# Kernel optimization log

Measured on AMD Instinct MI355X. Metric: run time of the kernel, lower is better.

The kernel has to match this reference:

```python
import jax, jax.numpy as jnp
import numpy as np

IN_F, OUT_F = 64, 32
N = IN_F * OUT_F + OUT_F  # 2080 sampled parameters (weights + bias)
B, S = 8, 2048
SCALE_INIT = 1.0 * float(np.sqrt(2.0 / (IN_F + OUT_F)))


def setup_inputs() -> dict:
    key = jax.random.key(0)
    k_x, k_eps, k_loc, k_cov = jax.random.split(key, 4)
    x = jax.random.normal(k_x, (B, S, IN_F), dtype=jnp.float32)
    eps = jax.random.normal(k_eps, (B, S, N), dtype=jnp.float32)
    loc = 0.01 * jax.random.normal(k_loc, (N,), dtype=jnp.float32)
    logvar = jnp.full((N,), float(np.log(SCALE_INIT)), dtype=jnp.float32)
    n_off = N * (N - 1) // 2
    cov_flat = 0.001 * jax.random.normal(k_cov, (n_off,), dtype=jnp.float32)
    return {"x": x, "eps": eps, "loc": loc, "logvar": logvar, "cov_flat": cov_flat}


def reference(x, eps, loc, logvar, cov_flat):
    n = loc.shape[0]
    in_f = x.shape[-1]
    out_f = n // (in_f + 1)  # n = out*(in+1)
    # flat_to_triangular (strictly lower) + make_cholesky, vectorized scatter
    rows, cols = np.tril_indices(n, -1)
    A = jnp.zeros((n, n), dtype=x.dtype).at[rows, cols].set(cov_flat)
    L = A + jnp.diag(jnp.exp(logvar * 0.5))  # off-diag from cov, diag = std
    # MultivariateNormal rsample: loc + L @ eps (per batch sample)
    W = loc + jnp.einsum('bsn,mn->bsm', eps, L)  # [B,S,N]
    b = W[..., :out_f]
    Wm = W[..., out_f:].reshape(*W.shape[:-1], in_f, out_f)  # [B,S,in,out]
    y = jnp.einsum('bsh,bshk->bsk', x, Wm) + b
    return y
```

## Files before the change

kernel.cpp:

```cpp
#include <hip/hip_runtime.h>
#include <hip/hip_bf16.h>

#define IN_F  64
#define OUT_F 32
#define NV    2080
#define NPAD  2176
#define MM    16384
#define KK    2080
#define NBN   17
#define BM    256

typedef __attribute__((ext_vector_type(4))) float f32x4;
typedef __bf16 bf16x8 __attribute__((ext_vector_type(8)));

using gas_ptr = const __attribute__((address_space(1))) void*;
using lds_ptr = __attribute__((address_space(3))) void*;

__global__ __launch_bounds__(256) void build_L_k(const float* __restrict__ cov,
                                                 const float* __restrict__ logvar,
                                                 __hip_bfloat16* __restrict__ LB) {
    const int idx = blockIdx.x * 256 + threadIdx.x;
    const int m = idx / KK;
    const int k = idx - m * KK;
    float v = 0.0f;
    if (m < NV) {
        if (k < m)       v = cov[(size_t)(m * (m - 1) / 2) + k];
        else if (k == m) v = expf(0.5f * logvar[m]);
    }
    LB[idx] = __float2bfloat16(v);
}

__global__ __launch_bounds__(256, 2) void gemm_v3_k(const float* __restrict__ A,
                                                    const __hip_bfloat16* __restrict__ BT,
                                                    const float* __restrict__ loc,
                                                    const float* __restrict__ x,
                                                    float* __restrict__ Ypart) {
    __shared__ __align__(16) __hip_bfloat16 As[2][BM * 32];
    __shared__ __align__(16) __hip_bfloat16 Bs[3][128 * 32];
    __shared__ float xs[BM][4];

    const int tid  = threadIdx.x;
    const int bm   = blockIdx.x;
    const int bn   = (NBN - 1) - blockIdx.y;
    const int wave = tid >> 6;
    const int lane = tid & 63;
    const int quad = lane >> 4;
    const int r16  = lane & 15;
    const int kblocks = min(KK / 32, 4 * bn + 4);

    {
        const int row = bm * BM + tid;
#pragma unroll
        for (int c = 0; c < 4; c++) {
            const int h = 4 * bn - 1 + c;
            float w = 0.0f;
            if (bn == 0 && c == 0)       w = 1.0f;
            else if (h >= 0 && h < IN_F) w = x[(size_t)row * IN_F + h];
            xs[tid][c] = w;
        }
    }

    const float*          __restrict__ Ag = A  + (size_t)bm * BM * KK;
    const __hip_bfloat16* __restrict__ Bg = BT + (size_t)bn * 128 * KK;

    size_t agofs[4]; int aldso[4];
#pragma unroll
    for (int u = 0; u < 4; u++) {
        const int c = tid + 256 * u;
        const int r = c >> 2, p = (c & 3) ^ ((r >> 1) & 3);
        agofs[u] = (size_t)r * KK + (size_t)(p * 8);
        aldso[u] = c * 8;
    }
    size_t bgofs[2]; int bldso[2];
#pragma unroll
    for (int u = 0; u < 2; u++) {
        const int c = tid + 256 * u;
        const int r = c >> 2, p = (c & 3) ^ ((r >> 1) & 3);
        bgofs[u] = (size_t)r * KK + (size_t)(p * 8);
        bldso[u] = c * 8;
    }

    int aofs[4], bofs[8];
#pragma unroll
    for (int i = 0; i < 4; i++) {
        const int arow = 64 * wave + 16 * i + r16;
        aofs[i] = arow * 32 + (quad ^ ((arow >> 1) & 3)) * 8;
    }
#pragma unroll
    for (int j = 0; j < 8; j++) {
        const int brow = 16 * j + r16;
        bofs[j] = brow * 32 + (quad ^ ((brow >> 1) & 3)) * 8;
    }

    f32x4 acc[4][8];
#pragma unroll
    for (int i = 0; i < 4; i++)
#pragma unroll
        for (int j = 0; j < 8; j++) acc[i][j] = f32x4{0.f, 0.f, 0.f, 0.f};

    f32x4 ra[8];

    auto loadA = [&](int t) __attribute__((always_inline)) {
        const size_t k0 = (size_t)t * 32;
#pragma unroll
        for (int u = 0; u < 4; u++) {
            ra[2 * u]     = *(const f32x4*)(Ag + k0 + agofs[u]);
            ra[2 * u + 1] = *(const f32x4*)(Ag + k0 + agofs[u] + 4);
        }
    };
    auto writeA = [&](int buf) __attribute__((always_inline)) {
#pragma unroll
        for (int u = 0; u < 4; u++) {
            bf16x8 w;
#pragma unroll
            for (int q = 0; q < 4; q++) {
                w[q]     = (__bf16)ra[2 * u][q];
                w[4 + q] = (__bf16)ra[2 * u + 1][q];
            }
            *(bf16x8*)(&As[buf][0] + aldso[u]) = w;
        }
    };
    auto stageB = [&](int t, int buf) __attribute__((always_inline)) {
        const size_t k0 = (size_t)t * 32;
#pragma unroll
        for (int u = 0; u < 2; u++)
            __builtin_amdgcn_global_load_lds((gas_ptr)(Bg + k0 + bgofs[u]),
                                             (lds_ptr)(&Bs[buf][0] + bldso[u]), 16, 0, 0);
    };

    loadA(0);
    __builtin_amdgcn_sched_barrier(0);
    stageB(0, 0);
    stageB(1, 1);
    __builtin_amdgcn_sched_barrier(0);
    writeA(0);
    loadA(1);
    __builtin_amdgcn_sched_barrier(0);
    asm volatile("s_waitcnt vmcnt(10)" ::: "memory");
    asm volatile("s_waitcnt lgkmcnt(0)" ::: "memory");
    __builtin_amdgcn_s_barrier();
    __builtin_amdgcn_sched_barrier(0);

    auto iter = [&](int t, int jlo) __attribute__((always_inline)) {
        const bool pfA = (t + 1 < kblocks);
        const bool pfB = (t + 2 < kblocks);
        if (pfB) stageB(t + 2, (t + 2) % 3);
        const __hip_bfloat16* as = &As[t & 1][0];
        const __hip_bfloat16* bs = &Bs[t % 3][0];
        bf16x8 af[4];
#pragma unroll
        for (int i = 0; i < 4; i++) af[i] = *(const bf16x8*)(as + aofs[i]);
        __builtin_amdgcn_s_setprio(1);
#pragma unroll
        for (int j = 0; j < 8; j++) {
            if (j >= jlo) {
                const bf16x8 bf = *(const bf16x8*)(bs + bofs[j]);
#pragma unroll
                for (int i = 0; i < 4; i++)
                    acc[i][j] = __builtin_amdgcn_mfma_f32_16x16x32_bf16(af[i], bf, acc[i][j], 0, 0, 0);
            }
        }
        __builtin_amdgcn_s_setprio(0);
        if (pfA) {
            if (pfB) { asm volatile("s_waitcnt vmcnt(2)" ::: "memory"); }
            else     { asm volatile("s_waitcnt vmcnt(0)" ::: "memory"); }
            writeA((t + 1) & 1);
            if (pfB) loadA(t + 2);
            asm volatile("s_waitcnt lgkmcnt(0)" ::: "memory");
            __builtin_amdgcn_s_barrier();
            __builtin_amdgcn_sched_barrier(0);
        }
    };

    const int t_full = min(kblocks, 4 * bn + 1);
    int t = 0;
    for (; t < t_full; ++t) iter(t, 0);
    for (; t < kblocks; ++t) iter(t, 2 * t - 8 * bn);

    float locv[8];
#pragma unroll
    for (int j = 0; j < 8; j++) {
        const int col = bn * 128 + 16 * j + r16;
        locv[j] = (col < NV) ? loc[col] : 0.0f;
    }

    float* yp = Ypart + ((size_t)bn * MM + (size_t)bm * BM) * OUT_F;
#pragma unroll
    for (int i = 0; i < 4; i++) {
#pragma unroll
        for (int r = 0; r < 4; r++) {
            const int tl = 64 * wave + 16 * i + 4 * quad + r;
            float v0 = 0.0f, v1 = 0.0f;
#pragma unroll
            for (int c = 0; c < 4; c++) {
                const float w = xs[tl][c];
                v0 += w * (acc[i][2 * c][r]     + locv[2 * c]);
                v1 += w * (acc[i][2 * c + 1][r] + locv[2 * c + 1]);
            }
            yp[(size_t)tl * OUT_F + r16]      = v0;
            yp[(size_t)tl * OUT_F + 16 + r16] = v1;
        }
    }
}

__global__ __launch_bounds__(256) void reduce_y_k(const float4* __restrict__ yp,
                                                  float4* __restrict__ y) {
    const size_t i = (size_t)blockIdx.x * 256 + threadIdx.x;
    float4 s = yp[i];
#pragma unroll
    for (int b = 1; b < NBN; b++) {
        float4 v = yp[i + (size_t)b * (MM * OUT_F / 4)];
        s.x += v.x; s.y += v.y; s.z += v.z; s.w += v.w;
    }
    y[i] = s;
}

extern "C" void kernel_launch(void* const* d_in, const int* in_sizes, int n_in,
                              void* d_out, int out_size, void* d_ws, size_t ws_size,
                              hipStream_t stream) {
    const float* x      = (const float*)d_in[0];
    const float* eps    = (const float*)d_in[1];
    const float* loc    = (const float*)d_in[2];
    const float* logvar = (const float*)d_in[3];
    const float* cov    = (const float*)d_in[4];
    float* y = (float*)d_out;

    char* ws = (char*)d_ws;
    const size_t lb_bytes = (size_t)NPAD * KK * 2;
    __hip_bfloat16* LB    = (__hip_bfloat16*)ws;
    float*          Ypart = (float*)(ws + lb_bytes);

    build_L_k<<<(NPAD * KK) / 256, 256, 0, stream>>>(cov, logvar, LB);
    gemm_v3_k<<<dim3(MM / BM, NBN), 256, 0, stream>>>(eps, LB, loc, x, Ypart);
    reduce_y_k<<<(MM * OUT_F / 4) / 256, 256, 0, stream>>>((const float4*)Ypart, (float4*)y);
}
```

Baseline: 315.6 us.

## Restructure GEMM to stream N-tiles per K-slice with fused x-weighted epilogue

After: 417.7 us. 32.3% more time.

```diff
diff --git a/kernel.cpp b/kernel.cpp
--- a/kernel.cpp
+++ b/kernel.cpp
@@ -7,7 +7,7 @@
 #define NPAD  2176
 #define MM    16384
 #define KK    2080
-#define NBN   17
+#define NTC   8
 #define BM    256
 
 typedef __attribute__((ext_vector_type(4))) float f32x4;
@@ -30,38 +30,23 @@
     LB[idx] = __float2bfloat16(v);
 }
 
-__global__ __launch_bounds__(256, 2) void gemm_v3_k(const float* __restrict__ A,
-                                                    const __hip_bfloat16* __restrict__ BT,
-                                                    const float* __restrict__ loc,
-                                                    const float* __restrict__ x,
-                                                    float* __restrict__ Ypart) {
+__global__ __launch_bounds__(256) void gemm_v4_k(const float* __restrict__ A,
+                                                 const __hip_bfloat16* __restrict__ BT,
+                                                 const float* __restrict__ loc,
+                                                 const float* __restrict__ x,
+                                                 float* __restrict__ Ypart) {
     __shared__ __align__(16) __hip_bfloat16 As[2][BM * 32];
-    __shared__ __align__(16) __hip_bfloat16 Bs[3][128 * 32];
-    __shared__ float xs[BM][4];
+    __shared__ __align__(16) __hip_bfloat16 Bs[2][128 * 32];
 
     const int tid  = threadIdx.x;
     const int bm   = blockIdx.x;
-    const int bn   = (NBN - 1) - blockIdx.y;
+    const int tc   = blockIdx.y;
     const int wave = tid >> 6;
     const int lane = tid & 63;
     const int quad = lane >> 4;
     const int r16  = lane & 15;
-    const int kblocks = min(KK / 32, 4 * bn + 4);
-
-    {
-        const int row = bm * BM + tid;
-#pragma unroll
-        for (int c = 0; c < 4; c++) {
-            const int h = 4 * bn - 1 + c;
-            float w = 0.0f;
-            if (bn == 0 && c == 0)       w = 1.0f;
-            else if (h >= 0 && h < IN_F) w = x[(size_t)row * IN_F + h];
-            xs[tid][c] = w;
-        }
-    }
-
-    const float*          __restrict__ Ag = A  + (size_t)bm * BM * KK;
-    const __hip_bfloat16* __restrict__ Bg = BT + (size_t)bn * 128 * KK;
+
+    const float* __restrict__ Ag = A + (size_t)bm * BM * KK;
 
     size_t agofs[4]; int aldso[4];
 #pragma unroll
@@ -92,11 +77,13 @@
         bofs[j] = brow * 32 + (quad ^ ((brow >> 1) & 3)) * 8;
     }
 
-    f32x4 acc[4][8];
-#pragma unroll
-    for (int i = 0; i < 4; i++)
-#pragma unroll
-        for (int j = 0; j < 8; j++) acc[i][j] = f32x4{0.f, 0.f, 0.f, 0.f};
+    int rowi[4];
+#pragma unroll
+    for (int i = 0; i < 4; i++) rowi[i] = bm * BM + 64 * wave + 16 * i + r16;
+
+    f32x4 yacc[4][2];
+#pragma unroll
+    for (int i = 0; i < 4; i++) { yacc[i][0] = f32x4{0.f,0.f,0.f,0.f}; yacc[i][1] = f32x4{0.f,0.f,0.f,0.f}; }
 
     f32x4 ra[8];
 
@@ -120,95 +107,128 @@
             *(bf16x8*)(&As[buf][0] + aldso[u]) = w;
         }
     };
-    auto stageB = [&](int t, int buf) __attribute__((always_inline)) {
-        const size_t k0 = (size_t)t * 32;
+    auto stageB = [&](int t, int bn, int buf) __attribute__((always_inline)) {
+        const __hip_bfloat16* Bg = BT + (size_t)bn * 128 * KK + (size_t)t * 32;
 #pragma unroll
         for (int u = 0; u < 2; u++)
-            __builtin_amdgcn_global_load_lds((gas_ptr)(Bg + k0 + bgofs[u]),
+            __builtin_amdgcn_global_load_lds((gas_ptr)(Bg + bgofs[u]),
                                              (lds_ptr)(&Bs[buf][0] + bldso[u]), 16, 0, 0);
     };
-
-    loadA(0);
-    __builtin_amdgcn_sched_barrier(0);
-    stageB(0, 0);
-    stageB(1, 1);
-    __builtin_amdgcn_sched_barrier(0);
+    auto loadW = [&](int bn, f32x4* w) __attribute__((always_inline)) {
+        if (bn == 0) {
+#pragma unroll
+            for (int i = 0; i < 4; i++) {
+                f32x4 v = *(const f32x4*)(x + (size_t)rowi[i] * IN_F);
+                w[i] = f32x4{1.0f, v[0], v[1], v[2]};
+            }
+        } else if (bn == 16) {
+#pragma unroll
+            for (int i = 0; i < 4; i++) {
+                float v = x[(size_t)rowi[i] * IN_F + 63];
+                w[i] = f32x4{v, 0.f, 0.f, 0.f};
+            }
+        } else {
+#pragma unroll
+            for (int i = 0; i < 4; i++)
+                w[i] = *(const f32x4*)(x + (size_t)rowi[i] * IN_F + 4 * bn - 1);
+        }
+    };
+
+    int t = tc, bn = tc >> 2;
+    loadA(t);
+    stageB(t, bn, 0);
+    f32x4 w[4];
+    loadW(bn, w);
     writeA(0);
-    loadA(1);
-    __builtin_amdgcn_sched_barrier(0);
-    asm volatile("s_waitcnt vmcnt(10)" ::: "memory");
+    asm volatile("s_waitcnt vmcnt(0)" ::: "memory");
     asm volatile("s_waitcnt lgkmcnt(0)" ::: "memory");
     __builtin_amdgcn_s_barrier();
     __builtin_amdgcn_sched_barrier(0);
 
-    auto iter = [&](int t, int jlo) __attribute__((always_inline)) {
-        const bool pfA = (t + 1 < kblocks);
-        const bool pfB = (t + 2 < kblocks);
-        if (pfB) stageB(t + 2, (t + 2) % 3);
-        const __hip_bfloat16* as = &As[t & 1][0];
-        const __hip_bfloat16* bs = &Bs[t % 3][0];
-        bf16x8 af[4];
-#pragma unroll
-        for (int i = 0; i < 4; i++) af[i] = *(const bf16x8*)(as + aofs[i]);
+    bf16x8 af[4];
+#pragma unroll
+    for (int i = 0; i < 4; i++) af[i] = *(const bf16x8*)(&As[0][0] + aofs[i]);
+    int abuf = 0, bbuf = 0;
+
+    for (;;) {
+        int t1, bn1; bool hasNext;
+        if (bn < 16) { t1 = t; bn1 = bn + 1; hasNext = true; }
+        else         { t1 = t + NTC; bn1 = t1 >> 2; hasNext = (t1 <= KK / 32 - 1); }
+        const bool stA = (bn == 16) && hasNext;
+
+        if (hasNext) stageB(t1, bn1, bbuf ^ 1);
+        f32x4 wn[4];
+        if (hasNext) loadW(bn1, wn);
+        if (stA) loadA(t1);
+
+        const bool addloc = (t == 0);
+        f32x4 lv[8];
+        if (addloc) {
+#pragma unroll
+            for (int j = 0; j < 8; j++) {
+                const int cb = 128 * bn + 16 * j + 4 * quad;
+                lv[j] = (cb < NV - 3) ? *(const f32x4*)(loc + cb) : f32x4{0.f,0.f,0.f,0.f};
+            }
+        }
+
+        const int jlo = (2 * t > 8 * bn) ? (2 * t - 8 * bn) : 0;
+        const __hip_bfloat16* bs = &Bs[bbuf][0];
         __builtin_amdgcn_s_setprio(1);
 #pragma unroll
         for (int j = 0; j < 8; j++) {
             if (j >= jlo) {
-                const bf16x8 bf = *(const bf16x8*)(bs + bofs[j]);
-#pragma unroll
-                for (int i = 0; i < 4; i++)
-                    acc[i][j] = __builtin_amdgcn_mfma_f32_16x16x32_bf16(af[i], bf, acc[i][j], 0, 0, 0);
+                const bf16x8 bfr = *(const bf16x8*)(bs + bofs[j]);
+#pragma unroll
+                for (int i = 0; i < 4; i++) {
+                    f32x4 tl = __builtin_amdgcn_mfma_f32_16x16x32_bf16(
+                                   bfr, af[i], f32x4{0.f,0.f,0.f,0.f}, 0, 0, 0);
+                    if (addloc) tl += lv[j];
+                    const float wc = w[i][j >> 1];
+                    yacc[i][j & 1] += wc * tl;
+                }
             }
         }
         __builtin_amdgcn_s_setprio(0);
-        if (pfA) {
-            if (pfB) { asm volatile("s_waitcnt vmcnt(2)" ::: "memory"); }
-            else     { asm volatile("s_waitcnt vmcnt(0)" ::: "memory"); }
-            writeA((t + 1) & 1);
-            if (pfB) loadA(t + 2);
-            asm volatile("s_waitcnt lgkmcnt(0)" ::: "memory");
-            __builtin_amdgcn_s_barrier();
-            __builtin_amdgcn_sched_barrier(0);
-        }
-    };
-
-    const int t_full = min(kblocks, 4 * bn + 1);
-    int t = 0;
-    for (; t < t_full; ++t) iter(t, 0);
-    for (; t < kblocks; ++t) iter(t, 2 * t - 8 * bn);
-
-    float locv[8];
-#pragma unroll
-    for (int j = 0; j < 8; j++) {
-        const int col = bn * 128 + 16 * j + r16;
-        locv[j] = (col < NV) ? loc[col] : 0.0f;
-    }
-
-    float* yp = Ypart + ((size_t)bn * MM + (size_t)bm * BM) * OUT_F;
+
+        if (!hasNext) break;
+
+        if (stA) {
+            asm volatile("s_waitcnt vmcnt(0)" ::: "memory");
+            writeA(abuf ^ 1);
+        } else {
+            asm volatile("s_waitcnt vmcnt(4)" ::: "memory");
+        }
+        asm volatile("s_waitcnt lgkmcnt(0)" ::: "memory");
+        __builtin_amdgcn_s_barrier();
+        __builtin_amdgcn_sched_barrier(0);
+
+        if (stA) {
+            abuf ^= 1;
+#pragma unroll
+            for (int i = 0; i < 4; i++) af[i] = *(const bf16x8*)(&As[abuf][0] + aofs[i]);
+        }
+        bbuf ^= 1;
+#pragma unroll
+        for (int i = 0; i < 4; i++) w[i] = wn[i];
+        t = t1; bn = bn1;
+    }
+
+    float* yp = Ypart + ((size_t)tc * MM + (size_t)bm * BM) * OUT_F;
 #pragma unroll
     for (int i = 0; i < 4; i++) {
-#pragma unroll
-        for (int r = 0; r < 4; r++) {
-            const int tl = 64 * wave + 16 * i + 4 * quad + r;
-            float v0 = 0.0f, v1 = 0.0f;
-#pragma unroll
-            for (int c = 0; c < 4; c++) {
-                const float w = xs[tl][c];
-                v0 += w * (acc[i][2 * c][r]     + locv[2 * c]);
-                v1 += w * (acc[i][2 * c + 1][r] + locv[2 * c + 1]);
-            }
-            yp[(size_t)tl * OUT_F + r16]      = v0;
-            yp[(size_t)tl * OUT_F + 16 + r16] = v1;
-        }
-    }
-}
-
-__global__ __launch_bounds__(256) void reduce_y_k(const float4* __restrict__ yp,
-                                                  float4* __restrict__ y) {
+        const int row = 64 * wave + 16 * i + r16;
+#pragma unroll
+        for (int d = 0; d < 2; d++)
+            *(f32x4*)(yp + (size_t)row * OUT_F + 16 * d + 4 * quad) = yacc[i][d];
+    }
+}
+
+__global__ __launch_bounds__(256) void reduce8_k(const float4* __restrict__ yp,
+                                                 float4* __restrict__ y) {
     const size_t i = (size_t)blockIdx.x * 256 + threadIdx.x;
     float4 s = yp[i];
 #pragma unroll
-    for (int b = 1; b < NBN; b++) {
+    for (int b = 1; b < NTC; b++) {
         float4 v = yp[i + (size_t)b * (MM * OUT_F / 4)];
         s.x += v.x; s.y += v.y; s.z += v.z; s.w += v.w;
     }
@@ -231,6 +251,6 @@
     float*          Ypart = (float*)(ws + lb_bytes);
 
     build_L_k<<<(NPAD * KK) / 256, 256, 0, stream>>>(cov, logvar, LB);
-    gemm_v3_k<<<dim3(MM / BM, NBN), 256, 0, stream>>>(eps, LB, loc, x, Ypart);
-    reduce_y_k<<<(MM * OUT_F / 4) / 256, 256, 0, stream>>>((const float4*)Ypart, (float4*)y);
-}
+    gemm_v4_k<<<dim3(MM / BM, NTC), 256, 0, stream>>>(eps, LB, loc, x, Ypart);
+    reduce8_k<<<(MM * OUT_F / 4) / 256, 256, 0, stream>>>((const float4*)Ypart, (float4*)y);
+}
```

## Load A fragments directly from global into registers, skipping LDS staging

Applied to the files above, without the earlier changes.

Measured after the change: 917.9 us. +190.8%, slower.

```diff
diff --git a/kernel.cpp b/kernel.cpp
--- a/kernel.cpp
+++ b/kernel.cpp
@@ -30,12 +30,11 @@
     LB[idx] = __float2bfloat16(v);
 }
 
-__global__ __launch_bounds__(256, 2) void gemm_v3_k(const float* __restrict__ A,
+__global__ __launch_bounds__(256, 2) void gemm_v5_k(const float* __restrict__ A,
                                                     const __hip_bfloat16* __restrict__ BT,
                                                     const float* __restrict__ loc,
                                                     const float* __restrict__ x,
                                                     float* __restrict__ Ypart) {
-    __shared__ __align__(16) __hip_bfloat16 As[2][BM * 32];
     __shared__ __align__(16) __hip_bfloat16 Bs[3][128 * 32];
     __shared__ float xs[BM][4];
 
@@ -63,14 +62,13 @@
     const float*          __restrict__ Ag = A  + (size_t)bm * BM * KK;
     const __hip_bfloat16* __restrict__ Bg = BT + (size_t)bn * 128 * KK;
 
-    size_t agofs[4]; int aldso[4];
-#pragma unroll
-    for (int u = 0; u < 4; u++) {
-        const int c = tid + 256 * u;
-        const int r = c >> 2, p = (c & 3) ^ ((r >> 1) & 3);
-        agofs[u] = (size_t)r * KK + (size_t)(p * 8);
-        aldso[u] = c * 8;
-    }
+    size_t arofs[4];
+#pragma unroll
+    for (int i = 0; i < 4; i++) {
+        const int row = 64 * wave + 16 * i + r16;
+        arofs[i] = (size_t)row * KK + (size_t)(quad * 8);
+    }
+
     size_t bgofs[2]; int bldso[2];
 #pragma unroll
     for (int u = 0; u < 2; u++) {
@@ -80,12 +78,7 @@
         bldso[u] = c * 8;
     }
 
-    int aofs[4], bofs[8];
-#pragma unroll
-    for (int i = 0; i < 4; i++) {
-        const int arow = 64 * wave + 16 * i + r16;
-        aofs[i] = arow * 32 + (quad ^ ((arow >> 1) & 3)) * 8;
-    }
+    int bofs[8];
 #pragma unroll
     for (int j = 0; j < 8; j++) {
         const int brow = 16 * j + r16;
@@ -98,75 +91,65 @@
 #pragma unroll
         for (int j = 0; j < 8; j++) acc[i][j] = f32x4{0.f, 0.f, 0.f, 0.f};
 
-    f32x4 ra[8];
-
-    auto loadA = [&](int t) __attribute__((always_inline)) {
-        const size_t k0 = (size_t)t * 32;
-#pragma unroll
-        for (int u = 0; u < 4; u++) {
-            ra[2 * u]     = *(const f32x4*)(Ag + k0 + agofs[u]);
-            ra[2 * u + 1] = *(const f32x4*)(Ag + k0 + agofs[u] + 4);
-        }
-    };
-    auto writeA = [&](int buf) __attribute__((always_inline)) {
-#pragma unroll
-        for (int u = 0; u < 4; u++) {
-            bf16x8 w;
-#pragma unroll
-            for (int q = 0; q < 4; q++) {
-                w[q]     = (__bf16)ra[2 * u][q];
-                w[4 + q] = (__bf16)ra[2 * u + 1][q];
-            }
-            *(bf16x8*)(&As[buf][0] + aldso[u]) = w;
+    f32x4 raA[8], raB[8];
+
+    auto loadA = [&](f32x4 (&r)[8], int t) __attribute__((always_inline)) {
+        const float* p = Ag + (size_t)t * 32;
+#pragma unroll
+        for (int i = 0; i < 4; i++) {
+            r[2 * i]     = *(const f32x4*)(p + arofs[i]);
+            r[2 * i + 1] = *(const f32x4*)(p + arofs[i] + 4);
         }
     };
     auto stageB = [&](int t, int buf) __attribute__((always_inline)) {
-        const size_t k0 = (size_t)t * 32;
+        const __hip_bfloat16* bp = Bg + (size_t)t * 32;
 #pragma unroll
         for (int u = 0; u < 2; u++)
-            __builtin_amdgcn_global_load_lds((gas_ptr)(Bg + k0 + bgofs[u]),
+            __builtin_amdgcn_global_load_lds((gas_ptr)(bp + bgofs[u]),
                                              (lds_ptr)(&Bs[buf][0] + bldso[u]), 16, 0, 0);
     };
 
-    loadA(0);
-    __builtin_amdgcn_sched_barrier(0);
     stageB(0, 0);
+    loadA(raA, 0);
     stageB(1, 1);
     __builtin_amdgcn_sched_barrier(0);
-    writeA(0);
-    loadA(1);
-    __builtin_amdgcn_sched_barrier(0);
-    asm volatile("s_waitcnt vmcnt(10)" ::: "memory");
     asm volatile("s_waitcnt lgkmcnt(0)" ::: "memory");
     __builtin_amdgcn_s_barrier();
     __builtin_amdgcn_sched_barrier(0);
 
-    auto iter = [&](int t, int jlo) __attribute__((always_inline)) {
+    auto iter = [&](int t, f32x4 (&cur)[8], f32x4 (&nxt)[8], int jlo)
+        __attribute__((always_inline)) {
         const bool pfA = (t + 1 < kblocks);
         const bool pfB = (t + 2 < kblocks);
+        if (pfA) loadA(nxt, t + 1);
         if (pfB) stageB(t + 2, (t + 2) % 3);
-        const __hip_bfloat16* as = &As[t & 1][0];
+        __builtin_amdgcn_sched_barrier(0);
+
+        bf16x8 af[4];
+#pragma unroll
+        for (int i = 0; i < 4; i++) {
+#pragma unroll
+            for (int q = 0; q < 4; q++) {
+                af[i][q]     = (__bf16)cur[2 * i][q];
+                af[i][4 + q] = (__bf16)cur[2 * i + 1][q];
+            }
+        }
         const __hip_bfloat16* bs = &Bs[t % 3][0];
-        bf16x8 af[4];
-#pragma unroll
-        for (int i = 0; i < 4; i++) af[i] = *(const bf16x8*)(as + aofs[i]);
         __builtin_amdgcn_s_setprio(1);
 #pragma unroll
         for (int j = 0; j < 8; j++) {
             if (j >= jlo) {
-                const bf16x8 bf = *(const bf16x8*)(bs + bofs[j]);
+                const bf16x8 bfr = *(const bf16x8*)(bs + bofs[j]);
 #pragma unroll
                 for (int i = 0; i < 4; i++)
-                    acc[i][j] = __builtin_amdgcn_mfma_f32_16x16x32_bf16(af[i], bf, acc[i][j], 0, 0, 0);
+                    acc[i][j] = __builtin_amdgcn_mfma_f32_16x16x32_bf16(af[i], bfr, acc[i][j], 0, 0, 0);
             }
         }
         __builtin_amdgcn_s_setprio(0);
+
         if (pfA) {
-            if (pfB) { asm volatile("s_waitcnt vmcnt(2)" ::: "memory"); }
-            else     { asm volatile("s_waitcnt vmcnt(0)" ::: "memory"); }
-            writeA((t + 1) & 1);
-            if (pfB) loadA(t + 2);
-            asm volatile("s_waitcnt lgkmcnt(0)" ::: "memory");
+            if (pfB) { asm volatile("s_waitcnt vmcnt(10)" ::: "memory"); }
+            else     { asm volatile("s_waitcnt vmcnt(8)"  ::: "memory"); }
             __builtin_amdgcn_s_barrier();
             __builtin_amdgcn_sched_barrier(0);
         }
@@ -174,8 +157,18 @@
 
     const int t_full = min(kblocks, 4 * bn + 1);
     int t = 0;
-    for (; t < t_full; ++t) iter(t, 0);
-    for (; t < kblocks; ++t) iter(t, 2 * t - 8 * bn);
+    for (; t + 1 < t_full; t += 2) {
+        iter(t,     raA, raB, 0);
+        iter(t + 1, raB, raA, 0);
+    }
+    {
+        bool useA = true;
+        for (; t < kblocks; ++t, useA = !useA) {
+            const int jl = (2 * t > 8 * bn) ? (2 * t - 8 * bn) : 0;
+            if (useA) iter(t, raA, raB, jl);
+            else      iter(t, raB, raA, jl);
+        }
+    }
 
     float locv[8];
 #pragma unroll
@@ -231,6 +224,6 @@
     float*          Ypart = (float*)(ws + lb_bytes);
 
     build_L_k<<<(NPAD * KK) / 256, 256, 0, stream>>>(cov, logvar, LB);
-    gemm_v3_k<<<dim3(MM / BM, NBN), 256, 0, stream>>>(eps, LB, loc, x, Ypart);
+    gemm_v5_k<<<dim3(MM / BM, NBN), 256, 0, stream>>>(eps, LB, loc, x, Ypart);
     reduce_y_k<<<(MM * OUT_F / 4) / 256, 256, 0, stream>>>((const float4*)Ypart, (float4*)y);
 }
```
